# Performance work log

Measured on AMD Instinct MI355X. Metric: run time of the kernel, lower is better.

The kernel has to match this reference:

```python
import jax, jax.numpy as jnp
import numpy as np

D_MODEL = 768
NUM_HEADS = 12
HEAD_DIM = D_MODEL // NUM_HEADS


def setup_inputs() -> dict:
    key = jax.random.key(0)
    ks = jax.random.split(key, 12)
    B, S = 4, 1024
    x = jax.random.normal(ks[0], (B, S, D_MODEL), dtype=jnp.float32)
    boxes = jax.random.uniform(ks[1], (B, S, 4), dtype=jnp.float32)
    s = 1.0 / np.sqrt(D_MODEL)
    Wq = jax.random.normal(ks[2], (D_MODEL, D_MODEL), dtype=jnp.float32) * s
    bq = jnp.zeros((D_MODEL,), dtype=jnp.float32)
    Wk = jax.random.normal(ks[3], (D_MODEL, D_MODEL), dtype=jnp.float32) * s
    bk = jnp.zeros((D_MODEL,), dtype=jnp.float32)
    Wv = jax.random.normal(ks[4], (D_MODEL, D_MODEL), dtype=jnp.float32) * s
    bv = jnp.zeros((D_MODEL,), dtype=jnp.float32)
    Wo = jax.random.normal(ks[5], (D_MODEL, D_MODEL), dtype=jnp.float32) * s
    bo = jnp.zeros((D_MODEL,), dtype=jnp.float32)
    spatial_bias = jax.random.normal(ks[6], (NUM_HEADS,), dtype=jnp.float32)
    return {"x": x, "boxes": boxes, "Wq": Wq, "bq": bq, "Wk": Wk, "bk": bk,
            "Wv": Wv, "bv": bv, "Wo": Wo, "bo": bo, "spatial_bias": spatial_bias}


def reference(x, boxes, Wq, bq, Wk, bk, Wv, bv, Wo, bo, spatial_bias):
    B, S, _ = x.shape
    H, Dh = NUM_HEADS, HEAD_DIM
    # projections -> [B, H, S, Dh]
    def proj(W, b):
        return (x @ W.T + b).reshape(B, S, H, Dh).transpose(0, 2, 1, 3)
    Q, K, V = proj(Wq, bq), proj(Wk, bk), proj(Wv, bv)
    scores = jnp.einsum('bhsd,bhtd->bhst', Q, K) / np.sqrt(Dh)
    # spatial bias from box-center pairwise distances
    centers = jnp.stack([(boxes[:, :, 0] + boxes[:, :, 2]) * 0.5,
                         (boxes[:, :, 1] + boxes[:, :, 3]) * 0.5], axis=-1)  # [B,S,2]
    diff = centers[:, :, None, :] - centers[:, None, :, :]                    # [B,S,S,2]
    dist = jnp.linalg.norm(diff, axis=-1)                                     # [B,S,S]
    bias = -dist[:, None, :, :] * spatial_bias[None, :, None, None]           # [B,H,S,S]
    attn = jax.nn.softmax(scores + bias, axis=-1)
    attended = jnp.einsum('bhst,bhtd->bhsd', attn, V)
    attended = attended.transpose(0, 2, 1, 3).reshape(B, S, H * Dh)
    return attended @ Wo.T + bo
```

## Files before the change

kernel.cpp:

```cpp
#include <hip/hip_runtime.h>
#include <stdint.h>

#define NHEADS 12
#define HDIM   64
#define NB     4
#define SQ     1024
#define DM     768
#define NROWS  (NB*SQ)
#define NWE    (DM*DM)
#define NXE    (NROWS*DM)

typedef __attribute__((ext_vector_type(8))) short short8;
typedef __attribute__((ext_vector_type(4))) float f32x4;

__device__ __forceinline__ unsigned short f2bf(float f) {
  union { float f; unsigned u; } v; v.f = f;
  return (unsigned short)((v.u + 0x7fffu + ((v.u >> 16) & 1u)) >> 16);
}

__device__ __forceinline__ unsigned pack2bf(float lo, float hi) {
  return (unsigned)f2bf(lo) | ((unsigned)f2bf(hi) << 16);
}

__device__ __forceinline__ void gload16(const void* g, void* l) {
  __builtin_amdgcn_global_load_lds((__attribute__((address_space(1))) void*)(void*)g,
                                   (__attribute__((address_space(3))) void*)l, 16, 0, 0);
}

__global__ __launch_bounds__(256) void prep_kernel(
    const float* __restrict__ x, const float* __restrict__ Wq, const float* __restrict__ Wk,
    const float* __restrict__ Wv, const float* __restrict__ Wo, const float* __restrict__ boxes,
    unsigned short* __restrict__ xb, unsigned short* __restrict__ wcat,
    unsigned short* __restrict__ wob, float2* __restrict__ centers) {
  int i = blockIdx.x * 256 + threadIdx.x;
  if (i < NXE) { xb[i] = f2bf(x[i]); return; }
  i -= NXE;
  if (i < NWE) {
    wcat[i]           = f2bf(Wq[i]);
    wcat[NWE + i]     = f2bf(Wk[i]);
    wcat[2 * NWE + i] = f2bf(Wv[i]);
    wob[i]            = f2bf(Wo[i]);
    return;
  }
  i -= NWE;
  if (i < NROWS) {
    float4 bx = ((const float4*)boxes)[i];
    centers[i] = make_float2((bx.x + bx.z) * 0.5f, (bx.y + bx.w) * 0.5f);
  }
}

template <int EPI>
__global__ __launch_bounds__(256, 2) void gemm_bt(
    const unsigned short* __restrict__ A, const unsigned short* __restrict__ Bw,
    int K, int tiles_n,
    const float* __restrict__ b0, const float* __restrict__ b1, const float* __restrict__ b2,
    unsigned short* __restrict__ outQ, unsigned short* __restrict__ outK,
    unsigned short* __restrict__ outVt, float* __restrict__ outF) {
  __shared__ unsigned short lA[128 * 32];
  __shared__ unsigned short lB[128 * 32];
  const int tid = threadIdx.x, wave = tid >> 6, lane = tid & 63;
  const int tm = blockIdx.x / tiles_n, tn = blockIdx.x % tiles_n;
  const int wr = wave >> 1, wc = wave & 1;
  const int g = lane >> 4, c16 = lane & 15, kb8 = g * 8;

  f32x4 acc[4][4];
#pragma unroll
  for (int m = 0; m < 4; m++)
#pragma unroll
    for (int n = 0; n < 4; n++) acc[m][n] = (f32x4){0.f, 0.f, 0.f, 0.f};

  const unsigned short* Abase = A + (size_t)tm * 128 * K;
  const unsigned short* Bbase = Bw + (size_t)tn * 128 * K;
  const int lin0 = wave * 1024 + lane * 16;
  const int row0 = lin0 >> 6, cb0 = lin0 & 63;
  const int lin1 = lin0 + 4096;
  const int row1 = lin1 >> 6, cb1 = lin1 & 63;

  for (int kt = 0; kt < K; kt += 32) {
    __syncthreads();
    gload16((const char*)(Abase + (size_t)row0 * K + kt) + cb0, (char*)lA + wave * 1024);
    gload16((const char*)(Abase + (size_t)row1 * K + kt) + cb1, (char*)lA + wave * 1024 + 4096);
    gload16((const char*)(Bbase + (size_t)row0 * K + kt) + cb0, (char*)lB + wave * 1024);
    gload16((const char*)(Bbase + (size_t)row1 * K + kt) + cb1, (char*)lB + wave * 1024 + 4096);
    __syncthreads();
    short8 a[4], b[4];
#pragma unroll
    for (int m = 0; m < 4; m++) a[m] = *(const short8*)&lA[(wr * 64 + m * 16 + c16) * 32 + kb8];
#pragma unroll
    for (int n = 0; n < 4; n++) b[n] = *(const short8*)&lB[(wc * 64 + n * 16 + c16) * 32 + kb8];
#pragma unroll
    for (int m = 0; m < 4; m++)
#pragma unroll
      for (int n = 0; n < 4; n++)
        acc[m][n] = __builtin_amdgcn_mfma_f32_16x16x32_bf16(a[m], b[n], acc[m][n], 0, 0, 0);
  }

#pragma unroll
  for (int m = 0; m < 4; m++) {
    const int gm0 = tm * 128 + wr * 64 + m * 16 + g * 4;
    const int bb = gm0 >> 10, ss0 = gm0 & 1023;
#pragma unroll
    for (int n = 0; n < 4; n++) {
      const int gn = tn * 128 + wc * 64 + n * 16 + c16;
      if (EPI == 0) {
        const int which = gn / DM, nn = gn - which * DM;
        const int h = nn >> 6, dh = nn & 63;
        const float bias = (which == 0 ? b0 : which == 1 ? b1 : b2)[nn];
        const float scale = (which == 0) ? 0.1803368801f : 1.0f;
        if (which == 2) {
          ushort4 pk;
          pk.x = f2bf(acc[m][n][0] + bias);
          pk.y = f2bf(acc[m][n][1] + bias);
          pk.z = f2bf(acc[m][n][2] + bias);
          pk.w = f2bf(acc[m][n][3] + bias);
          *(ushort4*)&outVt[(((size_t)bb * NHEADS + h) * HDIM + dh) * SQ + ss0] = pk;
        } else {
          unsigned short* dst = (which == 0 ? outQ : outK) + ((size_t)bb * NHEADS + h) * SQ * HDIM;
#pragma unroll
          for (int r = 0; r < 4; r++)
            dst[(size_t)(ss0 + r) * HDIM + dh] = f2bf((acc[m][n][r] + bias) * scale);
        }
      } else {
        const float bias = b0[gn];
#pragma unroll
        for (int r = 0; r < 4; r++)
          outF[(size_t)(gm0 + r) * DM + gn] = acc[m][n][r] + bias;
      }
    }
  }
}

#define KVB  128
#define PSTR 136
__global__ __launch_bounds__(256, 3) void attn_kernel(
    const unsigned short* __restrict__ Qb, const unsigned short* __restrict__ Kb,
    const unsigned short* __restrict__ Vt, const float2* __restrict__ centers,
    const float* __restrict__ sbias, unsigned short* __restrict__ attb) {
  __shared__ unsigned short lK[KVB * HDIM];
  __shared__ unsigned short lV[HDIM * KVB];
  __shared__ float2 lcent[KVB];
  __shared__ unsigned short plds[4][16 * PSTR];
  const int tid = threadIdx.x, wave = tid >> 6, lane = tid & 63;
  const int g = lane >> 4, c16 = lane & 15, kb8 = g * 8;
  const int bid = blockIdx.x;
  const int xcd = bid & 7, li = bid >> 3;
  const int bh = xcd * 6 + (li >> 4);
  const int qt = li & 15;
  const int b = bh / NHEADS, h = bh - b * NHEADS;
  const float sb = sbias[h] * 1.44269504f;

  const unsigned short* Qh = Qb + (size_t)bh * SQ * HDIM;
  const char* Kc = (const char*)(Kb + (size_t)bh * SQ * HDIM);
  const char* Vc = (const char*)(Vt + (size_t)bh * HDIM * SQ);
  const float2* cent_g = centers + b * SQ;

  const int l8 = lane >> 3, l7 = lane & 7;
  const int kLane = l8 * 128 + ((l7 * 16) ^ (l8 << 4));
  const int v16 = lane >> 4, m16 = lane & 15;

  const int q = qt * 64 + wave * 16 + c16;
  short8 qf[2];
  qf[0] = *(const short8*)&Qh[(size_t)q * HDIM + kb8];
  qf[1] = *(const short8*)&Qh[(size_t)q * HDIM + 32 + kb8];
  const float2 cq = cent_g[q];

  float mreg = -1e30f, lreg = 0.f;
  f32x4 oacc[4];
#pragma unroll
  for (int dd = 0; dd < 4; dd++) oacc[dd] = (f32x4){0.f, 0.f, 0.f, 0.f};

  const int swk = (c16 & 7) << 4;
#pragma unroll 1
  for (int tb = 0; tb < SQ; tb += KVB) {
    __syncthreads();
    {
      const char* kbase = Kc + (size_t)tb * 128;
#pragma unroll
      for (int j = 0; j < 4; j++) {
        const int i = wave * 4 + j;
        gload16(kbase + i * 1024 + kLane, (char*)lK + i * 1024);
      }
      const char* vbase = Vc + (size_t)tb * 2;
#pragma unroll
      for (int j = 0; j < 4; j++) {
        const int i = wave * 4 + j;
        const int row = i * 4 + v16;
        gload16(vbase + (size_t)row * 2048 + ((m16 * 16) ^ ((4 * (i & 1) + v16) << 4)),
                (char*)lV + i * 1024);
      }
      if (tid < KVB) lcent[tid] = cent_g[tb + tid];
    }
    __syncthreads();
    f32x4 sv[8];
#pragma unroll
    for (int cc = 0; cc < 8; cc++) {
      const int rb = (cc * 16 + c16) * 128;
      short8 k0 = *(const short8*)((const char*)lK + rb + ((g * 16) ^ swk));
      short8 k1 = *(const short8*)((const char*)lK + rb + ((64 + g * 16) ^ swk));
      f32x4 s = (f32x4){0.f, 0.f, 0.f, 0.f};
      s = __builtin_amdgcn_mfma_f32_16x16x32_bf16(k0, qf[0], s, 0, 0, 0);
      s = __builtin_amdgcn_mfma_f32_16x16x32_bf16(k1, qf[1], s, 0, 0, 0);
      sv[cc] = s;
    }
#pragma unroll
    for (int cc = 0; cc < 8; cc++) {
      const float4* cp = (const float4*)&lcent[cc * 16 + g * 4];
      float4 c01 = cp[0], c23 = cp[1];
      float dx, dy;
      dx = cq.x - c01.x; dy = cq.y - c01.y;
      sv[cc][0] -= __builtin_amdgcn_sqrtf(dx * dx + dy * dy) * sb;
      dx = cq.x - c01.z; dy = cq.y - c01.w;
      sv[cc][1] -= __builtin_amdgcn_sqrtf(dx * dx + dy * dy) * sb;
      dx = cq.x - c23.x; dy = cq.y - c23.y;
      sv[cc][2] -= __builtin_amdgcn_sqrtf(dx * dx + dy * dy) * sb;
      dx = cq.x - c23.z; dy = cq.y - c23.w;
      sv[cc][3] -= __builtin_amdgcn_sqrtf(dx * dx + dy * dy) * sb;
    }
    float lm = -1e30f;
#pragma unroll
    for (int cc = 0; cc < 8; cc++) {
      float a0 = fmaxf(sv[cc][0], sv[cc][1]), a1 = fmaxf(sv[cc][2], sv[cc][3]);
      lm = fmaxf(lm, fmaxf(a0, a1));
    }
    if (!__all(lm <= mreg + 8.0f)) {
      float vmax = fmaxf(lm, __shfl_xor(lm, 16));
      vmax = fmaxf(vmax, __shfl_xor(vmax, 32));
      const float mn = fmaxf(mreg, vmax);
      const float sc = __builtin_amdgcn_exp2f(mreg - mn);
      lreg *= sc;
#pragma unroll
      for (int dd = 0; dd < 4; dd++)
#pragma unroll
        for (int r = 0; r < 4; r++) oacc[dd][r] *= sc;
      mreg = mn;
    }
    float ps = 0.f;
#pragma unroll
    for (int cc = 0; cc < 8; cc++)
#pragma unroll
      for (int r = 0; r < 4; r++) {
        sv[cc][r] = __builtin_amdgcn_exp2f(sv[cc][r] - mreg);
        ps += sv[cc][r];
      }
    lreg += ps;
#pragma unroll
    for (int cc = 0; cc < 8; cc++) {
      uint2 u;
      u.x = pack2bf(sv[cc][0], sv[cc][1]);
      u.y = pack2bf(sv[cc][2], sv[cc][3]);
      *(uint2*)&plds[wave][c16 * PSTR + cc * 16 + g * 4] = u;
    }
#pragma unroll
    for (int kc = 0; kc < 4; kc++) {
      short8 pf = *(const short8*)&plds[wave][c16 * PSTR + kc * 32 + kb8];
#pragma unroll
      for (int dd = 0; dd < 4; dd++) {
        short8 vf = *(const short8*)((const char*)lV + (dd * 16 + c16) * 256 +
                                     ((kc * 64 + g * 16) ^ swk));
        oacc[dd] = __builtin_amdgcn_mfma_f32_16x16x32_bf16(vf, pf, oacc[dd], 0, 0, 0);
      }
    }
  }
  lreg += __shfl_xor(lreg, 16);
  lreg += __shfl_xor(lreg, 32);
  const float inv = 1.f / lreg;
#pragma unroll
  for (int dd = 0; dd < 4; dd++) {
    uint2 u;
    u.x = pack2bf(oacc[dd][0] * inv, oacc[dd][1] * inv);
    u.y = pack2bf(oacc[dd][2] * inv, oacc[dd][3] * inv);
    *(uint2*)&attb[(size_t)(b * SQ + q) * DM + h * HDIM + dd * 16 + g * 4] = u;
  }
}

extern "C" void kernel_launch(void* const* d_in, const int* in_sizes, int n_in,
                              void* d_out, int out_size, void* d_ws, size_t ws_size,
                              hipStream_t stream) {
  const float* x     = (const float*)d_in[0];
  const float* boxes = (const float*)d_in[1];
  const float* Wq    = (const float*)d_in[2];
  const float* bq    = (const float*)d_in[3];
  const float* Wk    = (const float*)d_in[4];
  const float* bk    = (const float*)d_in[5];
  const float* Wv    = (const float*)d_in[6];
  const float* bv    = (const float*)d_in[7];
  const float* Wo    = (const float*)d_in[8];
  const float* bo    = (const float*)d_in[9];
  const float* sb    = (const float*)d_in[10];

  char* ws = (char*)d_ws;
  unsigned short* xb   = (unsigned short*)(ws);
  unsigned short* wcat = (unsigned short*)(ws + 6291456);
  unsigned short* wob  = (unsigned short*)(ws + 9830400);
  unsigned short* qb   = (unsigned short*)(ws + 11010048);
  unsigned short* kb   = (unsigned short*)(ws + 17301504);
  unsigned short* vtb  = (unsigned short*)(ws + 23592960);
  unsigned short* attb = (unsigned short*)(ws + 29884416);
  float2* centers      = (float2*)(ws + 36175872);
  float* out = (float*)d_out;

  prep_kernel<<<14608, 256, 0, stream>>>(x, Wq, Wk, Wv, Wo, boxes, xb, wcat, wob, centers);
  gemm_bt<0><<<32 * 18, 256, 0, stream>>>(xb, wcat, DM, 18, bq, bk, bv, qb, kb, vtb, nullptr);
  attn_kernel<<<768, 256, 0, stream>>>(qb, kb, vtb, centers, sb, attb);
  gemm_bt<1><<<32 * 6, 256, 0, stream>>>(attb, wob, DM, 6, bo, nullptr, nullptr,
                                         nullptr, nullptr, nullptr, out);
}
```

Baseline: 96.95 us.

## Double-buffer LDS loads in GEMM and attention, retile output projection

Both GEMM and attention kernels now use double-buffered LDS stages. Each iteration drains the outstanding DMA, syncs, then issues the next tile's global-to-LDS loads before computing on the current one, so memory traffic overlaps MFMA work and one barrier per iteration is dropped. The attention KV block shrinks from 128 to 64 so two buffers fit, with new swizzled V staging. The output projection moves to 64x64 tiles, giving 768 blocks instead of 192 for better CU occupancy, at the cost of smaller per-block reuse.

```diff
diff --git a/kernel.cpp b/kernel.cpp
--- a/kernel.cpp
+++ b/kernel.cpp
@@ -25,6 +25,11 @@
 __device__ __forceinline__ void gload16(const void* g, void* l) {
   __builtin_amdgcn_global_load_lds((__attribute__((address_space(1))) void*)(void*)g,
                                    (__attribute__((address_space(3))) void*)l, 16, 0, 0);
+}
+
+__device__ __forceinline__ void drain_dma() {
+  asm volatile("s_waitcnt vmcnt(0)" ::: "memory");
+  __builtin_amdgcn_sched_barrier(0);
 }
 
 __global__ __launch_bounds__(256) void prep_kernel(
@@ -49,59 +54,72 @@
   }
 }
 
-template <int EPI>
+template <int EPI, int BM, int BN>
 __global__ __launch_bounds__(256, 2) void gemm_bt(
     const unsigned short* __restrict__ A, const unsigned short* __restrict__ Bw,
     int K, int tiles_n,
     const float* __restrict__ b0, const float* __restrict__ b1, const float* __restrict__ b2,
     unsigned short* __restrict__ outQ, unsigned short* __restrict__ outK,
     unsigned short* __restrict__ outVt, float* __restrict__ outF) {
-  __shared__ unsigned short lA[128 * 32];
-  __shared__ unsigned short lB[128 * 32];
+  constexpr int MF = BM / 32, NF = BN / 32;
+  __shared__ unsigned short lA[2][BM * 32];
+  __shared__ unsigned short lB[2][BN * 32];
   const int tid = threadIdx.x, wave = tid >> 6, lane = tid & 63;
   const int tm = blockIdx.x / tiles_n, tn = blockIdx.x % tiles_n;
   const int wr = wave >> 1, wc = wave & 1;
   const int g = lane >> 4, c16 = lane & 15, kb8 = g * 8;
 
-  f32x4 acc[4][4];
-#pragma unroll
-  for (int m = 0; m < 4; m++)
-#pragma unroll
-    for (int n = 0; n < 4; n++) acc[m][n] = (f32x4){0.f, 0.f, 0.f, 0.f};
-
-  const unsigned short* Abase = A + (size_t)tm * 128 * K;
-  const unsigned short* Bbase = Bw + (size_t)tn * 128 * K;
-  const int lin0 = wave * 1024 + lane * 16;
-  const int row0 = lin0 >> 6, cb0 = lin0 & 63;
-  const int lin1 = lin0 + 4096;
-  const int row1 = lin1 >> 6, cb1 = lin1 & 63;
-
-  for (int kt = 0; kt < K; kt += 32) {
+  f32x4 acc[MF][NF];
+#pragma unroll
+  for (int m = 0; m < MF; m++)
+#pragma unroll
+    for (int n = 0; n < NF; n++) acc[m][n] = (f32x4){0.f, 0.f, 0.f, 0.f};
+
+  const unsigned short* Abase = A + (size_t)tm * BM * K;
+  const unsigned short* Bbase = Bw + (size_t)tn * BN * K;
+  const int srow = lane >> 2, scb = (lane & 3) << 4;
+
+  auto stage = [&](int kt, int s) {
+#pragma unroll
+    for (int c = wave; c < BM / 16; c += 4)
+      gload16((const char*)(Abase + (size_t)(c * 16 + srow) * K + kt) + scb,
+              (char*)lA[s] + c * 1024);
+#pragma unroll
+    for (int c = wave; c < BN / 16; c += 4)
+      gload16((const char*)(Bbase + (size_t)(c * 16 + srow) * K + kt) + scb,
+              (char*)lB[s] + c * 1024);
+  };
+
+  stage(0, 0);
+  const int nk = K >> 5;
+#pragma unroll 1
+  for (int i = 0; i < nk; i++) {
+    drain_dma();
     __syncthreads();
-    gload16((const char*)(Abase + (size_t)row0 * K + kt) + cb0, (char*)lA + wave * 1024);
-    gload16((const char*)(Abase + (size_t)row1 * K + kt) + cb1, (char*)lA + wave * 1024 + 4096);
-    gload16((const char*)(Bbase + (size_t)row0 * K + kt) + cb0, (char*)lB + wave * 1024);
-    gload16((const char*)(Bbase + (size_t)row1 * K + kt) + cb1, (char*)lB + wave * 1024 + 4096);
-    __syncthreads();
-    short8 a[4], b[4];
-#pragma unroll
-    for (int m = 0; m < 4; m++) a[m] = *(const short8*)&lA[(wr * 64 + m * 16 + c16) * 32 + kb8];
-#pragma unroll
-    for (int n = 0; n < 4; n++) b[n] = *(const short8*)&lB[(wc * 64 + n * 16 + c16) * 32 + kb8];
-#pragma unroll
-    for (int m = 0; m < 4; m++)
-#pragma unroll
-      for (int n = 0; n < 4; n++)
+    if (i + 1 < nk) stage((i + 1) * 32, (i + 1) & 1);
+    const unsigned short* sA = lA[i & 1];
+    const unsigned short* sB = lB[i & 1];
+    short8 a[MF], b[NF];
+#pragma unroll
+    for (int m = 0; m < MF; m++)
+      a[m] = *(const short8*)&sA[(wr * (BM / 2) + m * 16 + c16) * 32 + kb8];
+#pragma unroll
+    for (int n = 0; n < NF; n++)
+      b[n] = *(const short8*)&sB[(wc * (BN / 2) + n * 16 + c16) * 32 + kb8];
+#pragma unroll
+    for (int m = 0; m < MF; m++)
+#pragma unroll
+      for (int n = 0; n < NF; n++)
         acc[m][n] = __builtin_amdgcn_mfma_f32_16x16x32_bf16(a[m], b[n], acc[m][n], 0, 0, 0);
   }
 
 #pragma unroll
-  for (int m = 0; m < 4; m++) {
-    const int gm0 = tm * 128 + wr * 64 + m * 16 + g * 4;
+  for (int m = 0; m < MF; m++) {
+    const int gm0 = tm * BM + wr * (BM / 2) + m * 16 + g * 4;
     const int bb = gm0 >> 10, ss0 = gm0 & 1023;
 #pragma unroll
-    for (int n = 0; n < 4; n++) {
-      const int gn = tn * 128 + wc * 64 + n * 16 + c16;
+    for (int n = 0; n < NF; n++) {
+      const int gn = tn * BN + wc * (BN / 2) + n * 16 + c16;
       if (EPI == 0) {
         const int which = gn / DM, nn = gn - which * DM;
         const int h = nn >> 6, dh = nn & 63;
@@ -130,15 +148,15 @@
   }
 }
 
-#define KVB  128
-#define PSTR 136
+#define KVB  64
+#define PSTR 72
 __global__ __launch_bounds__(256, 3) void attn_kernel(
     const unsigned short* __restrict__ Qb, const unsigned short* __restrict__ Kb,
     const unsigned short* __restrict__ Vt, const float2* __restrict__ centers,
     const float* __restrict__ sbias, unsigned short* __restrict__ attb) {
-  __shared__ unsigned short lK[KVB * HDIM];
-  __shared__ unsigned short lV[HDIM * KVB];
-  __shared__ float2 lcent[KVB];
+  __shared__ unsigned short lK[2][KVB * HDIM];
+  __shared__ unsigned short lV[2][HDIM * KVB];
+  __shared__ float2 lcent[2][KVB];
   __shared__ unsigned short plds[4][16 * PSTR];
   const int tid = threadIdx.x, wave = tid >> 6, lane = tid & 63;
   const int g = lane >> 4, c16 = lane & 15, kb8 = g * 8;
@@ -155,8 +173,23 @@
   const float2* cent_g = centers + b * SQ;
 
   const int l8 = lane >> 3, l7 = lane & 7;
-  const int kLane = l8 * 128 + ((l7 * 16) ^ (l8 << 4));
-  const int v16 = lane >> 4, m16 = lane & 15;
+  const int swizL = (l7 * 16) ^ (l8 << 4);
+
+  auto stage = [&](int tbn, int s) {
+    const char* kbase = Kc + (size_t)tbn * 128;
+#pragma unroll
+    for (int j = 0; j < 2; j++) {
+      const int i = wave * 2 + j;
+      gload16(kbase + i * 1024 + l8 * 128 + swizL, (char*)lK[s] + i * 1024);
+    }
+    const char* vbase = Vc + (size_t)tbn * 2;
+#pragma unroll
+    for (int j = 0; j < 2; j++) {
+      const int i = wave * 2 + j;
+      gload16(vbase + (size_t)(i * 8 + l8) * 2048 + swizL, (char*)lV[s] + i * 1024);
+    }
+    if (tid < KVB) lcent[s][tid] = cent_g[tbn + tid];
+  };
 
   const int q = qt * 64 + wave * 16 + c16;
   short8 qf[2];
@@ -169,42 +202,29 @@
 #pragma unroll
   for (int dd = 0; dd < 4; dd++) oacc[dd] = (f32x4){0.f, 0.f, 0.f, 0.f};
 
+  stage(0, 0);
+
   const int swk = (c16 & 7) << 4;
 #pragma unroll 1
-  for (int tb = 0; tb < SQ; tb += KVB) {
+  for (int t = 0; t < SQ / KVB; t++) {
+    const int cur = t & 1;
+    drain_dma();
     __syncthreads();
-    {
-      const char* kbase = Kc + (size_t)tb * 128;
-#pragma unroll
-      for (int j = 0; j < 4; j++) {
-        const int i = wave * 4 + j;
-        gload16(kbase + i * 1024 + kLane, (char*)lK + i * 1024);
-      }
-      const char* vbase = Vc + (size_t)tb * 2;
-#pragma unroll
-      for (int j = 0; j < 4; j++) {
-        const int i = wave * 4 + j;
-        const int row = i * 4 + v16;
-        gload16(vbase + (size_t)row * 2048 + ((m16 * 16) ^ ((4 * (i & 1) + v16) << 4)),
-                (char*)lV + i * 1024);
-      }
-      if (tid < KVB) lcent[tid] = cent_g[tb + tid];
-    }
-    __syncthreads();
-    f32x4 sv[8];
-#pragma unroll
-    for (int cc = 0; cc < 8; cc++) {
+    if (t + 1 < SQ / KVB) stage((t + 1) * KVB, cur ^ 1);
+    f32x4 sv[4];
+#pragma unroll
+    for (int cc = 0; cc < 4; cc++) {
       const int rb = (cc * 16 + c16) * 128;
-      short8 k0 = *(const short8*)((const char*)lK + rb + ((g * 16) ^ swk));
-      short8 k1 = *(const short8*)((const char*)lK + rb + ((64 + g * 16) ^ swk));
+      short8 k0 = *(const short8*)((const char*)lK[cur] + rb + ((g * 16) ^ swk));
+      short8 k1 = *(const short8*)((const char*)lK[cur] + rb + ((64 + g * 16) ^ swk));
       f32x4 s = (f32x4){0.f, 0.f, 0.f, 0.f};
       s = __builtin_amdgcn_mfma_f32_16x16x32_bf16(k0, qf[0], s, 0, 0, 0);
       s = __builtin_amdgcn_mfma_f32_16x16x32_bf16(k1, qf[1], s, 0, 0, 0);
       sv[cc] = s;
     }
 #pragma unroll
-    for (int cc = 0; cc < 8; cc++) {
-      const float4* cp = (const float4*)&lcent[cc * 16 + g * 4];
+    for (int cc = 0; cc < 4; cc++) {
+      const float4* cp = (const float4*)&lcent[cur][cc * 16 + g * 4];
       float4 c01 = cp[0], c23 = cp[1];
       float dx, dy;
       dx = cq.x - c01.x; dy = cq.y - c01.y;
@@ -218,7 +238,7 @@
     }
     float lm = -1e30f;
 #pragma unroll
-    for (int cc = 0; cc < 8; cc++) {
+    for (int cc = 0; cc < 4; cc++) {
       float a0 = fmaxf(sv[cc][0], sv[cc][1]), a1 = fmaxf(sv[cc][2], sv[cc][3]);
       lm = fmaxf(lm, fmaxf(a0, a1));
     }
@@ -236,7 +256,7 @@
     }
     float ps = 0.f;
 #pragma unroll
-    for (int cc = 0; cc < 8; cc++)
+    for (int cc = 0; cc < 4; cc++)
 #pragma unroll
       for (int r = 0; r < 4; r++) {
         sv[cc][r] = __builtin_amdgcn_exp2f(sv[cc][r] - mreg);
@@ -244,18 +264,18 @@
       }
     lreg += ps;
 #pragma unroll
-    for (int cc = 0; cc < 8; cc++) {
+    for (int cc = 0; cc < 4; cc++) {
       uint2 u;
       u.x = pack2bf(sv[cc][0], sv[cc][1]);
       u.y = pack2bf(sv[cc][2], sv[cc][3]);
       *(uint2*)&plds[wave][c16 * PSTR + cc * 16 + g * 4] = u;
     }
 #pragma unroll
-    for (int kc = 0; kc < 4; kc++) {
+    for (int kc = 0; kc < 2; kc++) {
       short8 pf = *(const short8*)&plds[wave][c16 * PSTR + kc * 32 + kb8];
 #pragma unroll
       for (int dd = 0; dd < 4; dd++) {
-        short8 vf = *(const short8*)((const char*)lV + (dd * 16 + c16) * 256 +
+        short8 vf = *(const short8*)((const char*)lV[cur] + (dd * 16 + c16) * 128 +
                                      ((kc * 64 + g * 16) ^ swk));
         oacc[dd] = __builtin_amdgcn_mfma_f32_16x16x32_bf16(vf, pf, oacc[dd], 0, 0, 0);
       }
@@ -300,8 +320,9 @@
   float* out = (float*)d_out;
 
   prep_kernel<<<14608, 256, 0, stream>>>(x, Wq, Wk, Wv, Wo, boxes, xb, wcat, wob, centers);
-  gemm_bt<0><<<32 * 18, 256, 0, stream>>>(xb, wcat, DM, 18, bq, bk, bv, qb, kb, vtb, nullptr);
+  gemm_bt<0, 128, 128><<<32 * 18, 256, 0, stream>>>(xb, wcat, DM, 18, bq, bk, bv,
+                                                    qb, kb, vtb, nullptr);
   attn_kernel<<<768, 256, 0, stream>>>(qb, kb, vtb, centers, sb, attb);
-  gemm_bt<1><<<32 * 6, 256, 0, stream>>>(attb, wob, DM, 6, bo, nullptr, nullptr,
-                                         nullptr, nullptr, nullptr, out);
-}
+  gemm_bt<1, 64, 64><<<64 * 12, 256, 0, stream>>>(attb, wob, DM, 12, bo, nullptr, nullptr,
+                                                  nullptr, nullptr, nullptr, out);
+}
```

Result: faster. 93.76 us (-3.3%).
